# Optimization experiments

Hardware: AMD Instinct MI355X
Metric: run time of the kernel (lower is better)

The kernel has to match this reference:

```python
import jax, jax.numpy as jnp
import numpy as np

HEAD = 2

def setup_inputs() -> dict:
    key = jax.random.key(0)
    ks = jax.random.split(key, 12)
    B, C, H, W = 4, 512, 64, 64
    IC = 256
    N = H * W
    s = 0.02
    return {
        "x": jax.random.normal(ks[0], (B, C, H, W), jnp.float32),
        "output_attn": jax.random.normal(ks[1], (B, C, H, W), jnp.float32),
        "mlp_w": jax.random.normal(ks[2], (N, N), jnp.float32) * s,
        "mlp_b": jax.random.normal(ks[3], (N,), jnp.float32) * s,
        "g_w": jax.random.normal(ks[4], (IC, C), jnp.float32) * s,
        "g_b": jax.random.normal(ks[5], (IC,), jnp.float32) * s,
        "theta_w": jax.random.normal(ks[6], (IC, C), jnp.float32) * s,
        "theta_b": jax.random.normal(ks[7], (IC,), jnp.float32) * s,
        "phi_w": jax.random.normal(ks[8], (IC, C), jnp.float32) * s,
        "phi_b": jax.random.normal(ks[9], (IC,), jnp.float32) * s,
        "out_w": jax.random.normal(ks[10], (C, IC), jnp.float32) * s,
        "out_b": jax.random.normal(ks[11], (C,), jnp.float32) * s,
    }

def _conv1x1(feat, w, b):
    # feat: [B, Cin, N], w: [Cout, Cin], b: [Cout] -> [B, Cout, N]
    return jnp.einsum('bcn,oc->bon', feat, w) + b[None, :, None]

def reference(x, output_attn, mlp_w, mlp_b, g_w, g_b, theta_w, theta_b,
              phi_w, phi_b, out_w, out_b):
    B, C, H, W = x.shape
    N = H * W
    IC = g_w.shape[0]
    d = IC // HEAD  # per-head dim

    xf = x.reshape(B, C, N)
    # head-MLP remix: only hd==HEAD slice is non-empty (integer-division bug in source)
    xf = xf + (jnp.einsum('bcn,mn->bcm', xf, mlp_w) + mlp_b)

    g = _conv1x1(xf, g_w, g_b)                       # [B, IC, N]
    g = g.reshape(B * HEAD, d, N).transpose(0, 2, 1)  # [BH, N, d]

    oa = output_attn.reshape(B, C, N)
    th = _conv1x1(oa, theta_w, theta_b).reshape(B * HEAD, d, N).transpose(0, 2, 1)  # [BH, N, d]
    ph = _conv1x1(xf, phi_w, phi_b).reshape(B * HEAD, d, N)                          # [BH, d, N]

    scale = 1.0 / (d ** 0.5)
    attn = jax.nn.softmax(jnp.einsum('bnd,bdm->bnm', th, ph) * scale, axis=-1)  # [BH, N, N]
    y = jnp.einsum('bnm,bmd->bnd', attn, g)           # [BH, N, d]
    y = y.reshape(B, HEAD, N, d).transpose(0, 2, 1, 3).reshape(B, N, IC)
    y = y.transpose(0, 2, 1)                          # [B, IC, N]

    out = output_attn + _conv1x1(y, out_w, out_b).reshape(B, C, H, W)
    return out
```

## Files before the change

### kernel.cpp

```cpp
#include <hip/hip_runtime.h>

typedef unsigned short us;
typedef us s8v __attribute__((ext_vector_type(8)));
typedef us s4v __attribute__((ext_vector_type(4)));
typedef float f4v __attribute__((ext_vector_type(4)));
typedef float f16v __attribute__((ext_vector_type(16)));
typedef __bf16 b2v __attribute__((ext_vector_type(2)));

static __device__ __forceinline__ us f2b(float f) {
  return __builtin_bit_cast(us, (__bf16)f);
}
static __device__ __forceinline__ unsigned f2b2(float lo, float hi) {
  b2v v = {(__bf16)lo, (__bf16)hi};
  return __builtin_bit_cast(unsigned, v);
}
static __device__ __forceinline__ float b2f(us s) {
  unsigned u = ((unsigned)s) << 16;
  return __builtin_bit_cast(float, u);
}

#define GLDS(src, dst)                                                        \
  __builtin_amdgcn_global_load_lds(                                           \
      (const __attribute__((address_space(1))) unsigned int*)(src),           \
      (__attribute__((address_space(3))) unsigned int*)(dst), 16, 0, 0)

__global__ __launch_bounds__(256) void castk(const float* __restrict__ in,
                                             us* __restrict__ out, int n4) {
  int i = blockIdx.x * 256 + threadIdx.x;
  int stride = gridDim.x * 256;
  for (; i < n4; i += stride) {
    float4 v = ((const float4*)in)[i];
    s4v s = {f2b(v.x), f2b(v.y), f2b(v.z), f2b(v.w)};
    ((s4v*)out)[i] = s;
  }
}

__global__ __launch_bounds__(256) void wcast4(const float* __restrict__ s0, us* __restrict__ o0,
                                              const float* __restrict__ s1, us* __restrict__ o1,
                                              const float* __restrict__ s2, us* __restrict__ o2,
                                              const float* __restrict__ s3, us* __restrict__ o3) {
  const float* s; us* o;
  int y = blockIdx.y;
  if (y == 0) { s = s0; o = o0; }
  else if (y == 1) { s = s1; o = o1; }
  else if (y == 2) { s = s2; o = o2; }
  else { s = s3; o = o3; }
  int i = blockIdx.x * 256 + threadIdx.x;
  for (; i < 32768; i += 8192) {
    float4 v = ((const float4*)s)[i];
    s4v r = {f2b(v.x), f2b(v.y), f2b(v.z), f2b(v.w)};
    ((s4v*)o)[i] = r;
  }
}

__global__ __launch_bounds__(256) void tcast(const float* __restrict__ in,
                                             us* __restrict__ out, int R, int C,
                                             us* __restrict__ out2) {
  __shared__ float t[64][65];
  const int tid = threadIdx.x;
  const long r0 = (long)blockIdx.y * 64, c0 = (long)blockIdx.x * 64;
#pragma unroll
  for (int j = 0; j < 4; ++j) {
    int idx = j * 256 + tid;
    int row = idx >> 4, c4 = (idx & 15) * 4;
    float4 v = *(const float4*)(in + (r0 + row) * C + c0 + c4);
    t[row][c4] = v.x; t[row][c4 + 1] = v.y; t[row][c4 + 2] = v.z; t[row][c4 + 3] = v.w;
    if (out2) {
      s4v s = {f2b(v.x), f2b(v.y), f2b(v.z), f2b(v.w)};
      *(s4v*)(out2 + (r0 + row) * C + c0 + c4) = s;
    }
  }
  __syncthreads();
#pragma unroll
  for (int j = 0; j < 4; ++j) {
    int idx = j * 256 + tid;
    int orow = idx >> 4, r4 = (idx & 15) * 4;
    s4v s = {f2b(t[r4][orow]), f2b(t[r4 + 1][orow]), f2b(t[r4 + 2][orow]), f2b(t[r4 + 3][orow])};
    *(s4v*)(out + (c0 + orow) * R + r0 + r4) = s;
  }
}

#define SW(row, kb) ((row) * 128 + ((kb) ^ (((row) & 7) << 4)))

template <int EPI, int AF32, int BF32, int SWZ, int DUAL>
__global__ __launch_bounds__(256) void gemm_nt(
    const void* __restrict__ Av, const void* __restrict__ Bv,
    int lda, int ldb, int K, long aZ, long bZ,
    const float* __restrict__ bias,
    const us* __restrict__ addb16,
    const float* __restrict__ addf32,
    us* __restrict__ outb16,
    float* __restrict__ outf32,
    const void* __restrict__ Av2,
    const void* __restrict__ Bv2,
    const float* __restrict__ bias2,
    us* __restrict__ outb16_2) {
  __shared__ __align__(16) us lA2[2][128 * 64];
  __shared__ __align__(16) us lB2[2][128 * 64];
  const int tid = threadIdx.x, l = tid & 63;
  const int lr = l & 15, lg = l >> 4;
  const int w = tid >> 6, wr = w >> 1, wc = w & 1;
  int bm, bn;
  if constexpr (SWZ) {
    int flat = blockIdx.y * gridDim.x + blockIdx.x;
    int re = (flat & 7) * ((gridDim.x * gridDim.y) >> 3) + (flat >> 3);
    bm = re % gridDim.x; bn = re / gridDim.x;
  } else { bm = blockIdx.x; bn = blockIdx.y; }
  int z = blockIdx.z;
  const void* Au = Av; const void* Bu = Bv;
  const float* biasu = bias; us* outu = outb16;
  if constexpr (DUAL) {
    if (z >= 4) { Au = Av2; Bu = Bv2; biasu = bias2; outu = outb16_2; z -= 4; }
  }
  const f4v zero = {0.f, 0.f, 0.f, 0.f};
  f4v acc[4][4];
#pragma unroll
  for (int i = 0; i < 4; ++i)
#pragma unroll
    for (int j = 0; j < 4; ++j) acc[i][j] = zero;

  int rS[4], cS[4];
#pragma unroll
  for (int j = 0; j < 4; ++j) {
    int byte = j * 4096 + tid * 16;
    rS[j] = byte >> 7;
    cS[j] = (byte & 127) ^ ((rS[j] & 7) << 4);
  }
  const char* Ab = (const char*)Au + ((long)z * aZ + (long)bm * 128 * lda) * 2;
  const char* Bb = (const char*)Bu + ((long)z * bZ + (long)bn * 128 * ldb) * 2;

  auto stage = [&](int bufi, int k0) {
    char* lab = (char*)lA2[bufi];
    char* lbb = (char*)lB2[bufi];
#pragma unroll
    for (int j = 0; j < 4; ++j) {
      if constexpr (AF32) {
        int byte = j * 4096 + tid * 16;
        int row = byte >> 7, kb = byte & 127;
        const float* af = (const float*)Au + (long)z * aZ + (long)(bm * 128 + row) * lda + k0 + (kb >> 1);
        float4 v0 = *(const float4*)af, v1 = *(const float4*)(af + 4);
        s8v va = {f2b(v0.x), f2b(v0.y), f2b(v0.z), f2b(v0.w), f2b(v1.x), f2b(v1.y), f2b(v1.z), f2b(v1.w)};
        *(s8v*)(lab + SW(row, kb)) = va;
      } else {
        GLDS(Ab + (long)rS[j] * lda * 2 + k0 * 2 + cS[j], lab + j * 4096 + w * 1024);
      }
      if constexpr (BF32) {
        int byte = j * 4096 + tid * 16;
        int row = byte >> 7, kb = byte & 127;
        const float* bf_ = (const float*)Bu + (long)z * bZ + (long)(bn * 128 + row) * ldb + k0 + (kb >> 1);
        float4 v0 = *(const float4*)bf_, v1 = *(const float4*)(bf_ + 4);
        s8v vb = {f2b(v0.x), f2b(v0.y), f2b(v0.z), f2b(v0.w), f2b(v1.x), f2b(v1.y), f2b(v1.z), f2b(v1.w)};
        *(s8v*)(lbb + SW(row, kb)) = vb;
      } else {
        GLDS(Bb + (long)rS[j] * ldb * 2 + k0 * 2 + cS[j], lbb + j * 4096 + w * 1024);
      }
    }
  };

  stage(0, 0);
  for (int k0 = 0; k0 < K; k0 += 64) {
    const int cur = (k0 >> 6) & 1;
    __syncthreads();
    if (k0 + 64 < K) stage(cur ^ 1, k0 + 64);
    const char* lab = (const char*)lA2[cur];
    const char* lbb = (const char*)lB2[cur];
#pragma unroll
    for (int ks = 0; ks < 2; ++ks) {
      s8v af[4], bf[4];
      const int kb = ks * 64 + lg * 16;
#pragma unroll
      for (int mi = 0; mi < 4; ++mi) {
        int row = wr * 64 + mi * 16 + lr;
        af[mi] = *(const s8v*)(lab + SW(row, kb));
      }
#pragma unroll
      for (int ni = 0; ni < 4; ++ni) {
        int row = wc * 64 + ni * 16 + lr;
        bf[ni] = *(const s8v*)(lbb + SW(row, kb));
      }
#pragma unroll
      for (int mi = 0; mi < 4; ++mi)
#pragma unroll
        for (int ni = 0; ni < 4; ++ni)
          acc[mi][ni] = __builtin_amdgcn_mfma_f32_16x16x32_bf16(af[mi], bf[ni], acc[mi][ni], 0, 0, 0);
    }
  }

#pragma unroll
  for (int mi = 0; mi < 4; ++mi) {
#pragma unroll
    for (int ni = 0; ni < 4; ++ni) {
#pragma unroll
      for (int r = 0; r < 4; ++r) {
        int row = bm * 128 + wr * 64 + mi * 16 + lg * 4 + r;
        int col = bn * 128 + wc * 64 + ni * 16 + lr;
        float v = acc[mi][ni][r];
        if constexpr (EPI == 0) {
          long idx = (long)row * 2048 + col;
          outu[idx] = f2b(v + b2f(addb16[idx]) + biasu[row]);
        } else if constexpr (EPI == 1) {
          long idx = ((long)(z * 2 + (col >> 7)) * 4096 + row) * 128 + (col & 127);
          outu[idx] = f2b(v + biasu[col]);
        } else if constexpr (EPI == 2) {
          long idx = ((long)(z * 256 + row)) * 4096 + col;
          outu[idx] = f2b(v + biasu[row]);
        } else {
          long idx = ((long)(z * 512 + row)) * 4096 + col;
          outf32[idx] = v + biasu[row] + addf32[idx];
        }
      }
    }
  }
}

__global__ __launch_bounds__(256, 2) void attn_k(const us* __restrict__ th,
                                                 const us* __restrict__ pht,
                                                 const us* __restrict__ g,
                                                 us* __restrict__ pY,
                                                 float* __restrict__ lml) {
  __shared__ __align__(16) us ph2[2][64 * 128];
  __shared__ __align__(16) us g2[2][128 * 64];
  const int tid = threadIdx.x, l = tid & 63, w = tid >> 6;
  const int l31 = l & 31, h = l >> 5;
  const int swz = (l31 & 7) << 4;
  const int flat = blockIdx.y * 32 + blockIdx.x;
  const int bh = flat & 7, rest = flat >> 3;
  const int half = rest & 1, qb = rest >> 1;
  const int b = bh >> 1, head = bh & 1;
  const int m00 = half * 2048;
  const float C1 = 0.12751802f;
  const f16v zero16 = {0.f};

  const char* phsrc = (const char*)(pht + (long)bh * 4096 * 128);
  const char* gsrc = (const char*)(g + (long)(b * 256 + head * 128) * 4096);

  int koff[4], voff[4];
#pragma unroll
  for (int j = 0; j < 4; ++j) {
    int d = j * 4096 + tid * 16;
    koff[j] = d ^ (((d >> 8) & 7) << 4);
    int rowg = d >> 7, kbg = d & 127;
    voff[j] = rowg * 8192 + (kbg ^ ((rowg & 7) << 4));
  }

  s8v qf[8];
  {
    const us* thp = th + ((long)bh * 4096 + qb * 128 + w * 32 + l31) * 128 + h * 8;
#pragma unroll
    for (int ks = 0; ks < 8; ++ks) qf[ks] = *(const s8v*)(thp + ks * 16);
  }

  f16v acc0 = zero16, acc1 = zero16, acc2 = zero16, acc3 = zero16;
  float l_run = 0.f;

  auto stage = [&](int bufi, int m0) {
    char* dk = (char*)ph2[bufi] + w * 1024;
    char* dv = (char*)g2[bufi] + w * 1024;
    const char* sk = phsrc + (long)m0 * 256;
    const char* sv = gsrc + (long)m0 * 2;
#pragma unroll
    for (int j = 0; j < 4; ++j) {
      GLDS(sk + koff[j], dk + j * 4096);
      GLDS(sv + voff[j], dv + j * 4096);
    }
  };

  stage(0, m00);
  __syncthreads();

  for (int t = 0; t < 32; ++t) {
    const int cur = t & 1;
    stage(cur ^ 1, m00 + ((t + 1) & 31) * 64);
    const char* phb = (const char*)ph2[cur];
    const char* gb = (const char*)g2[cur];

    f16v sA[2] = {zero16, zero16};
    __builtin_amdgcn_s_setprio(1);
#pragma unroll
    for (int ks = 0; ks < 8; ++ks) {
#pragma unroll
      for (int mt = 0; mt < 2; ++mt) {
        s8v kf = *(const s8v*)(phb + (mt * 32 + l31) * 256 + (((ks * 32) + h * 16) ^ swz));
        sA[mt] = __builtin_amdgcn_mfma_f32_32x32x16_bf16(kf, qf[ks], sA[mt], 0, 0, 0);
      }
    }
    __builtin_amdgcn_s_setprio(0);

    float sum = 0.f;
    s8v bfrag[4];
#pragma unroll
    for (int mt = 0; mt < 2; ++mt) {
#pragma unroll
      for (int k1 = 0; k1 < 2; ++k1) {
        const int base = k1 * 8;
        float p0 = __builtin_amdgcn_exp2f(sA[mt][base + 0] * C1);
        float p1 = __builtin_amdgcn_exp2f(sA[mt][base + 1] * C1);
        float p2 = __builtin_amdgcn_exp2f(sA[mt][base + 2] * C1);
        float p3 = __builtin_amdgcn_exp2f(sA[mt][base + 3] * C1);
        float p4 = __builtin_amdgcn_exp2f(sA[mt][base + 4] * C1);
        float p5 = __builtin_amdgcn_exp2f(sA[mt][base + 5] * C1);
        float p6 = __builtin_amdgcn_exp2f(sA[mt][base + 6] * C1);
        float p7 = __builtin_amdgcn_exp2f(sA[mt][base + 7] * C1);
        sum += ((p0 + p1) + (p2 + p3)) + ((p4 + p5) + (p6 + p7));
        unsigned E0 = f2b2(p0, p1), E1 = f2b2(p2, p3);
        unsigned O0 = f2b2(p4, p5), O1 = f2b2(p6, p7);
        asm("v_permlane32_swap_b32 %0, %1" : "+v"(E0), "+v"(O0));
        asm("v_permlane32_swap_b32 %0, %1" : "+v"(E1), "+v"(O1));
        uint4 u = {E0, E1, O0, O1};
        bfrag[mt * 2 + k1] = __builtin_bit_cast(s8v, u);
      }
    }
    sum += __shfl_xor(sum, 32, 64);
    l_run += sum;

    __builtin_amdgcn_s_setprio(1);
#pragma unroll
    for (int ks2 = 0; ks2 < 4; ++ks2) {
      const int kb = ((ks2 * 32) + h * 16) ^ swz;
      s8v v0 = *(const s8v*)(gb + (l31) * 128 + kb);
      s8v v1 = *(const s8v*)(gb + (32 + l31) * 128 + kb);
      s8v v2 = *(const s8v*)(gb + (64 + l31) * 128 + kb);
      s8v v3 = *(const s8v*)(gb + (96 + l31) * 128 + kb);
      acc0 = __builtin_amdgcn_mfma_f32_32x32x16_bf16(v0, bfrag[ks2], acc0, 0, 0, 0);
      acc1 = __builtin_amdgcn_mfma_f32_32x32x16_bf16(v1, bfrag[ks2], acc1, 0, 0, 0);
      acc2 = __builtin_amdgcn_mfma_f32_32x32x16_bf16(v2, bfrag[ks2], acc2, 0, 0, 0);
      acc3 = __builtin_amdgcn_mfma_f32_32x32x16_bf16(v3, bfrag[ks2], acc3, 0, 0, 0);
    }
    __builtin_amdgcn_s_setprio(0);

    __syncthreads();
  }

  const long gq = (long)bh * 4096 + qb * 128 + w * 32 + l31;
  if (h == 0) lml[gq * 2 + half] = l_run;
  us* py = pY + (gq * 2 + half) * 128;
#pragma unroll
  for (int gi = 0; gi < 4; ++gi) {
    int r0 = gi * 4;
    {
      uint2 u = {f2b2(acc0[r0], acc0[r0 + 1]), f2b2(acc0[r0 + 2], acc0[r0 + 3])};
      *(uint2*)(py + gi * 8 + 4 * h) = u;
    }
    {
      uint2 u = {f2b2(acc1[r0], acc1[r0 + 1]), f2b2(acc1[r0 + 2], acc1[r0 + 3])};
      *(uint2*)(py + 32 + gi * 8 + 4 * h) = u;
    }
    {
      uint2 u = {f2b2(acc2[r0], acc2[r0 + 1]), f2b2(acc2[r0 + 2], acc2[r0 + 3])};
      *(uint2*)(py + 64 + gi * 8 + 4 * h) = u;
    }
    {
      uint2 u = {f2b2(acc3[r0], acc3[r0 + 1]), f2b2(acc3[r0 + 2], acc3[r0 + 3])};
      *(uint2*)(py + 96 + gi * 8 + 4 * h) = u;
    }
  }
}

__global__ __launch_bounds__(256) void mergek(const us* __restrict__ pY,
                                              const float* __restrict__ lml,
                                              us* __restrict__ yt) {
  int idx = blockIdx.x * 256 + threadIdx.x;
  int gq = idx >> 4, dd8 = (idx & 15) * 8;
  float inv = 1.0f / (lml[gq * 2 + 0] + lml[gq * 2 + 1]);
  const us* base = pY + (long)gq * 256 + dd8;
  s8v Y0 = *(const s8v*)(base);
  s8v Y1 = *(const s8v*)(base + 128);
  s8v o;
#pragma unroll
  for (int i = 0; i < 8; ++i) o[i] = f2b((b2f(Y0[i]) + b2f(Y1[i])) * inv);
  int bh = gq >> 12, q = gq & 4095, b = bh >> 1, head = bh & 1;
  *(s8v*)(yt + ((long)b * 4096 + q) * 256 + head * 128 + dd8) = o;
}

extern "C" void kernel_launch(void* const* d_in, const int* in_sizes, int n_in,
                              void* d_out, int out_size, void* d_ws, size_t ws_size,
                              hipStream_t stream) {
  (void)in_sizes; (void)n_in; (void)out_size;
  const float* x       = (const float*)d_in[0];
  const float* oa      = (const float*)d_in[1];
  const float* mlp_w   = (const float*)d_in[2];
  const float* mlp_b   = (const float*)d_in[3];
  const float* g_w     = (const float*)d_in[4];
  const float* g_b     = (const float*)d_in[5];
  const float* theta_w = (const float*)d_in[6];
  const float* theta_b = (const float*)d_in[7];
  const float* phi_w   = (const float*)d_in[8];
  const float* phi_b   = (const float*)d_in[9];
  const float* out_w   = (const float*)d_in[10];
  const float* out_b   = (const float*)d_in[11];
  float* out = (float*)d_out;
  char* ws = (char*)d_ws;

  us* xf_t   = (us*)(ws + 0L);
  us* pY     = (us*)(ws + 0L);
  us* oat    = (us*)(ws + 16777216L);
  float* lml = (float*)(ws + 16777216L);
  us* xt     = (us*)(ws + 33554432L);
  us* g_ws   = (us*)(ws + 33554432L);
  us* th_ws  = (us*)(ws + 41943040L);
  us* xc     = (us*)(ws + 50331648L);
  us* ph_ws  = (us*)(ws + 50331648L);
  us* yt     = (us*)(ws + 58720256L);
  us* g_wb   = (us*)(ws + 67108864L);
  us* th_wb  = (us*)(ws + 67371008L);
  us* ph_wb  = (us*)(ws + 67633152L);
  us* out_wb = (us*)(ws + 67895296L);
  us* mlp_wb = (us*)(ws + 68157440L);
  const bool big = ws_size >= 101711872ULL;

  wcast4<<<dim3(32, 4), dim3(256), 0, stream>>>(g_w, g_wb, theta_w, th_wb,
                                                phi_w, ph_wb, out_w, out_wb);
  tcast<<<dim3(64, 32), dim3(256), 0, stream>>>(x, xt, 2048, 4096, xc);
  tcast<<<dim3(64, 32), dim3(256), 0, stream>>>(oa, oat, 2048, 4096, nullptr);

  if (big) {
    castk<<<dim3(1024), dim3(256), 0, stream>>>(mlp_w, mlp_wb, 4194304);
    gemm_nt<0, 0, 0, 1, 0><<<dim3(32, 16, 1), dim3(256), 0, stream>>>(
        mlp_wb, xc, 4096, 4096, 4096, 0, 0, mlp_b, xt, nullptr, xf_t, nullptr,
        nullptr, nullptr, nullptr, nullptr);
  } else {
    gemm_nt<0, 1, 0, 1, 0><<<dim3(32, 16, 1), dim3(256), 0, stream>>>(
        mlp_w, xc, 4096, 4096, 4096, 0, 0, mlp_b, xt, nullptr, xf_t, nullptr,
        nullptr, nullptr, nullptr, nullptr);
  }

  gemm_nt<1, 0, 0, 0, 1><<<dim3(32, 2, 8), dim3(256), 0, stream>>>(
      oat, th_wb, 2048, 512, 512, 512, 0, theta_b, nullptr, nullptr, th_ws, nullptr,
      xf_t, ph_wb, phi_b, ph_ws);
  gemm_nt<2, 0, 0, 0, 0><<<dim3(2, 32, 4), dim3(256), 0, stream>>>(
      g_wb, xf_t, 512, 2048, 512, 0, 512, g_b, nullptr, nullptr, g_ws, nullptr,
      nullptr, nullptr, nullptr, nullptr);

  attn_k<<<dim3(32, 16), dim3(256), 0, stream>>>(th_ws, ph_ws, g_ws, pY, lml);
  mergek<<<dim3(2048), dim3(256), 0, stream>>>(pY, lml, yt);

  gemm_nt<3, 0, 0, 0, 0><<<dim3(4, 32, 4), dim3(256), 0, stream>>>(
      out_wb, yt, 256, 256, 256, 0, 1048576L, out_b, nullptr, oa, nullptr, out,
      nullptr, nullptr, nullptr, nullptr);
}
```

Baseline: 247.6 us.

## Split attention keys four ways with smaller key tiles and higher occupancy

The attention kernel now splits the key range into four partitions of 1024 instead of two of 2048. Each iteration handles a 32-key tile instead of a 64-key tile, which halves shared-memory use and lets launch bounds request four blocks per CU. The grid doubles to 1024 blocks so more waves can hide latency. In exchange, the merge kernel must read and combine four partial outputs and four row sums, which doubles the partial-result traffic, and each tile does less MFMA work per barrier.

```diff
diff --git a/kernel.cpp b/kernel.cpp
--- a/kernel.cpp
+++ b/kernel.cpp
@@ -213,34 +213,34 @@
   }
 }
 
-__global__ __launch_bounds__(256, 2) void attn_k(const us* __restrict__ th,
+__global__ __launch_bounds__(256, 4) void attn_k(const us* __restrict__ th,
                                                  const us* __restrict__ pht,
                                                  const us* __restrict__ g,
                                                  us* __restrict__ pY,
                                                  float* __restrict__ lml) {
-  __shared__ __align__(16) us ph2[2][64 * 128];
-  __shared__ __align__(16) us g2[2][128 * 64];
+  __shared__ __align__(16) us ph2[2][32 * 128];
+  __shared__ __align__(16) us g2[2][128 * 32];
   const int tid = threadIdx.x, l = tid & 63, w = tid >> 6;
   const int l31 = l & 31, h = l >> 5;
   const int swz = (l31 & 7) << 4;
-  const int flat = blockIdx.y * 32 + blockIdx.x;
+  const int flat = blockIdx.y * 128 + blockIdx.x;
   const int bh = flat & 7, rest = flat >> 3;
-  const int half = rest & 1, qb = rest >> 1;
+  const int split = rest & 3, qb = rest >> 2;
   const int b = bh >> 1, head = bh & 1;
-  const int m00 = half * 2048;
+  const int m00 = split * 1024;
   const float C1 = 0.12751802f;
   const f16v zero16 = {0.f};
 
   const char* phsrc = (const char*)(pht + (long)bh * 4096 * 128);
   const char* gsrc = (const char*)(g + (long)(b * 256 + head * 128) * 4096);
 
-  int koff[4], voff[4];
-#pragma unroll
-  for (int j = 0; j < 4; ++j) {
+  int koff[2], voff[2];
+#pragma unroll
+  for (int j = 0; j < 2; ++j) {
     int d = j * 4096 + tid * 16;
     koff[j] = d ^ (((d >> 8) & 7) << 4);
-    int rowg = d >> 7, kbg = d & 127;
-    voff[j] = rowg * 8192 + (kbg ^ ((rowg & 7) << 4));
+    int dprow = d >> 7, dw = (d & 127) ^ ((dprow & 7) << 4);
+    voff[j] = (dprow * 2 + (dw >> 6)) * 8192 + (dw & 63);
   }
 
   s8v qf[8];
@@ -259,7 +259,7 @@
     const char* sk = phsrc + (long)m0 * 256;
     const char* sv = gsrc + (long)m0 * 2;
 #pragma unroll
-    for (int j = 0; j < 4; ++j) {
+    for (int j = 0; j < 2; ++j) {
       GLDS(sk + koff[j], dk + j * 4096);
       GLDS(sv + voff[j], dv + j * 4096);
     }
@@ -270,57 +270,59 @@
 
   for (int t = 0; t < 32; ++t) {
     const int cur = t & 1;
-    stage(cur ^ 1, m00 + ((t + 1) & 31) * 64);
+    stage(cur ^ 1, m00 + ((t + 1) & 31) * 32);
     const char* phb = (const char*)ph2[cur];
     const char* gb = (const char*)g2[cur];
 
-    f16v sA[2] = {zero16, zero16};
+    f16v sA = zero16;
     __builtin_amdgcn_s_setprio(1);
 #pragma unroll
     for (int ks = 0; ks < 8; ++ks) {
-#pragma unroll
-      for (int mt = 0; mt < 2; ++mt) {
-        s8v kf = *(const s8v*)(phb + (mt * 32 + l31) * 256 + (((ks * 32) + h * 16) ^ swz));
-        sA[mt] = __builtin_amdgcn_mfma_f32_32x32x16_bf16(kf, qf[ks], sA[mt], 0, 0, 0);
-      }
+      s8v kf = *(const s8v*)(phb + l31 * 256 + (((ks * 32) + h * 16) ^ swz));
+      sA = __builtin_amdgcn_mfma_f32_32x32x16_bf16(kf, qf[ks], sA, 0, 0, 0);
     }
     __builtin_amdgcn_s_setprio(0);
 
     float sum = 0.f;
-    s8v bfrag[4];
-#pragma unroll
-    for (int mt = 0; mt < 2; ++mt) {
-#pragma unroll
-      for (int k1 = 0; k1 < 2; ++k1) {
-        const int base = k1 * 8;
-        float p0 = __builtin_amdgcn_exp2f(sA[mt][base + 0] * C1);
-        float p1 = __builtin_amdgcn_exp2f(sA[mt][base + 1] * C1);
-        float p2 = __builtin_amdgcn_exp2f(sA[mt][base + 2] * C1);
-        float p3 = __builtin_amdgcn_exp2f(sA[mt][base + 3] * C1);
-        float p4 = __builtin_amdgcn_exp2f(sA[mt][base + 4] * C1);
-        float p5 = __builtin_amdgcn_exp2f(sA[mt][base + 5] * C1);
-        float p6 = __builtin_amdgcn_exp2f(sA[mt][base + 6] * C1);
-        float p7 = __builtin_amdgcn_exp2f(sA[mt][base + 7] * C1);
-        sum += ((p0 + p1) + (p2 + p3)) + ((p4 + p5) + (p6 + p7));
-        unsigned E0 = f2b2(p0, p1), E1 = f2b2(p2, p3);
-        unsigned O0 = f2b2(p4, p5), O1 = f2b2(p6, p7);
-        asm("v_permlane32_swap_b32 %0, %1" : "+v"(E0), "+v"(O0));
-        asm("v_permlane32_swap_b32 %0, %1" : "+v"(E1), "+v"(O1));
-        uint4 u = {E0, E1, O0, O1};
-        bfrag[mt * 2 + k1] = __builtin_bit_cast(s8v, u);
-      }
+    s8v bfrag[2];
+#pragma unroll
+    for (int k1 = 0; k1 < 2; ++k1) {
+      const int base = k1 * 8;
+      float p0 = __builtin_amdgcn_exp2f(sA[base + 0] * C1);
+      float p1 = __builtin_amdgcn_exp2f(sA[base + 1] * C1);
+      float p2 = __builtin_amdgcn_exp2f(sA[base + 2] * C1);
+      float p3 = __builtin_amdgcn_exp2f(sA[base + 3] * C1);
+      float p4 = __builtin_amdgcn_exp2f(sA[base + 4] * C1);
+      float p5 = __builtin_amdgcn_exp2f(sA[base + 5] * C1);
+      float p6 = __builtin_amdgcn_exp2f(sA[base + 6] * C1);
+      float p7 = __builtin_amdgcn_exp2f(sA[base + 7] * C1);
+      sum += ((p0 + p1) + (p2 + p3)) + ((p4 + p5) + (p6 + p7));
+      unsigned E0 = f2b2(p0, p1), E1 = f2b2(p2, p3);
+      unsigned O0 = f2b2(p4, p5), O1 = f2b2(p6, p7);
+      asm("v_permlane32_swap_b32 %0, %1" : "+v"(E0), "+v"(O0));
+      asm("v_permlane32_swap_b32 %0, %1" : "+v"(E1), "+v"(O1));
+      uint4 u = {E0, E1, O0, O1};
+      bfrag[k1] = __builtin_bit_cast(s8v, u);
     }
     sum += __shfl_xor(sum, 32, 64);
     l_run += sum;
 
     __builtin_amdgcn_s_setprio(1);
 #pragma unroll
-    for (int ks2 = 0; ks2 < 4; ++ks2) {
-      const int kb = ((ks2 * 32) + h * 16) ^ swz;
-      s8v v0 = *(const s8v*)(gb + (l31) * 128 + kb);
-      s8v v1 = *(const s8v*)(gb + (32 + l31) * 128 + kb);
-      s8v v2 = *(const s8v*)(gb + (64 + l31) * 128 + kb);
-      s8v v3 = *(const s8v*)(gb + (96 + l31) * 128 + kb);
+    for (int ks2 = 0; ks2 < 2; ++ks2) {
+      const int kb = ks2 * 32 + h * 16;
+      const int lo6 = (l31 & 1) << 6;
+#pragma unroll
+      for (int d0 = 0; d0 < 4; ++d0) {
+      }
+      int pr0 = (l31 >> 1);
+      s8v v0 = *(const s8v*)(gb + (pr0) * 128 + ((lo6 | kb) ^ ((pr0 & 7) << 4)));
+      int pr1 = 16 + (l31 >> 1);
+      s8v v1 = *(const s8v*)(gb + (pr1) * 128 + ((lo6 | kb) ^ ((pr1 & 7) << 4)));
+      int pr2 = 32 + (l31 >> 1);
+      s8v v2 = *(const s8v*)(gb + (pr2) * 128 + ((lo6 | kb) ^ ((pr2 & 7) << 4)));
+      int pr3 = 48 + (l31 >> 1);
+      s8v v3 = *(const s8v*)(gb + (pr3) * 128 + ((lo6 | kb) ^ ((pr3 & 7) << 4)));
       acc0 = __builtin_amdgcn_mfma_f32_32x32x16_bf16(v0, bfrag[ks2], acc0, 0, 0, 0);
       acc1 = __builtin_amdgcn_mfma_f32_32x32x16_bf16(v1, bfrag[ks2], acc1, 0, 0, 0);
       acc2 = __builtin_amdgcn_mfma_f32_32x32x16_bf16(v2, bfrag[ks2], acc2, 0, 0, 0);
@@ -332,8 +334,8 @@
   }
 
   const long gq = (long)bh * 4096 + qb * 128 + w * 32 + l31;
-  if (h == 0) lml[gq * 2 + half] = l_run;
-  us* py = pY + (gq * 2 + half) * 128;
+  if (h == 0) lml[gq * 4 + split] = l_run;
+  us* py = pY + (gq * 4 + split) * 128;
 #pragma unroll
   for (int gi = 0; gi < 4; ++gi) {
     int r0 = gi * 4;
@@ -361,13 +363,17 @@
                                               us* __restrict__ yt) {
   int idx = blockIdx.x * 256 + threadIdx.x;
   int gq = idx >> 4, dd8 = (idx & 15) * 8;
-  float inv = 1.0f / (lml[gq * 2 + 0] + lml[gq * 2 + 1]);
-  const us* base = pY + (long)gq * 256 + dd8;
+  float4 lv = *(const float4*)(lml + (long)gq * 4);
+  float inv = 1.0f / (lv.x + lv.y + lv.z + lv.w);
+  const us* base = pY + (long)gq * 512 + dd8;
   s8v Y0 = *(const s8v*)(base);
   s8v Y1 = *(const s8v*)(base + 128);
+  s8v Y2 = *(const s8v*)(base + 256);
+  s8v Y3 = *(const s8v*)(base + 384);
   s8v o;
 #pragma unroll
-  for (int i = 0; i < 8; ++i) o[i] = f2b((b2f(Y0[i]) + b2f(Y1[i])) * inv);
+  for (int i = 0; i < 8; ++i)
+    o[i] = f2b(((b2f(Y0[i]) + b2f(Y1[i])) + (b2f(Y2[i]) + b2f(Y3[i]))) * inv);
   int bh = gq >> 12, q = gq & 4095, b = bh >> 1, head = bh & 1;
   *(s8v*)(yt + ((long)b * 4096 + q) * 256 + head * 128 + dd8) = o;
 }
@@ -394,7 +400,6 @@
   us* xf_t   = (us*)(ws + 0L);
   us* pY     = (us*)(ws + 0L);
   us* oat    = (us*)(ws + 16777216L);
-  float* lml = (float*)(ws + 16777216L);
   us* xt     = (us*)(ws + 33554432L);
   us* g_ws   = (us*)(ws + 33554432L);
   us* th_ws  = (us*)(ws + 41943040L);
@@ -402,6 +407,7 @@
   us* ph_ws  = (us*)(ws + 50331648L);
   us* yt     = (us*)(ws + 58720256L);
   us* g_wb   = (us*)(ws + 67108864L);
+  float* lml = (float*)(ws + 67108864L);
   us* th_wb  = (us*)(ws + 67371008L);
   us* ph_wb  = (us*)(ws + 67633152L);
   us* out_wb = (us*)(ws + 67895296L);
@@ -431,7 +437,7 @@
       g_wb, xf_t, 512, 2048, 512, 0, 512, g_b, nullptr, nullptr, g_ws, nullptr,
       nullptr, nullptr, nullptr, nullptr);
 
-  attn_k<<<dim3(32, 16), dim3(256), 0, stream>>>(th_ws, ph_ws, g_ws, pY, lml);
+  attn_k<<<dim3(128, 8), dim3(256), 0, stream>>>(th_ws, ph_ws, g_ws, pY, lml);
   mergek<<<dim3(2048), dim3(256), 0, stream>>>(pY, lml, yt);
 
   gemm_nt<3, 0, 0, 0, 0><<<dim3(4, 32, 4), dim3(256), 0, stream>>>(
```

Result: slower. 306.1 us (+23.6%).
